# Optimization experiments

Measured on AMD Instinct MI355X. Metric: run time of the kernel, lower is better.

## Reference

```python
import jax, jax.numpy as jnp
import numpy as np

N = 100000   # num nodes
D = 128      # node_emb_dim
R = 8        # num_relations
E = 1600000  # num edges


def setup_inputs() -> dict:
    key = jax.random.key(0)
    k0, k1, k2, k3, k4 = jax.random.split(key, 5)
    x = jax.random.normal(k0, (N, D), dtype=jnp.float32)
    edge_index = jax.random.randint(k1, (2, E), 0, N, dtype=jnp.int32)
    edge_type = jax.random.randint(k2, (E,), 0, R, dtype=jnp.int32)
    scale = 1.0 / np.sqrt(D)
    W = (jax.random.normal(k3, (R, D, D), dtype=jnp.float32) * scale)       # per-relation weight
    W_root = (jax.random.normal(k4, (D, D), dtype=jnp.float32) * scale)     # root (self-loop) weight
    bias = jnp.zeros((D,), dtype=jnp.float32)
    return {"x": x, "W": W, "W_root": W_root, "bias": bias,
            "edge_index": edge_index, "edge_type": edge_type}


def reference(x, W, W_root, bias, edge_index, edge_type):
    # PyG RGCNConv (num_bases=None, aggr='mean', root_weight=True, bias=True):
    # out_i = x_i @ W_root + bias + sum_r mean_{j in N_r(i)} x_j @ W_r
    # Mean aggregation is linear, so aggregate neighbor features per (node, relation)
    # first, then apply the per-relation transform (avoids [E,D,D] intermediates).
    src, dst = edge_index[0], edge_index[1]
    seg = dst * R + edge_type                                   # [E] segment id per (dst, rel)
    cnt = jax.ops.segment_sum(jnp.ones((E,), x.dtype), seg, num_segments=N * R)  # [N*R]
    sums = jax.ops.segment_sum(x[src], seg, num_segments=N * R)                   # [N*R, D]
    mean = sums / jnp.maximum(cnt, 1.0)[:, None]                                  # [N*R, D]
    rel_out = jnp.einsum('nrd,rde->ne', mean.reshape(N, R, D), W)                 # [N, D]
    return rel_out + x @ W_root + bias
```

## Files before the change

### kernel.cpp

```cpp
#include <hip/hip_runtime.h>


constexpr int D = 128;
constexpr int R = 8;
constexpr int TILE = 2048;
constexpr int CW = 64;
constexpr int LDA = 40;

typedef __bf16 bf16x8 __attribute__((ext_vector_type(8)));
typedef float  f32x4  __attribute__((ext_vector_type(4)));
typedef unsigned short u16x8 __attribute__((ext_vector_type(8)));
typedef unsigned short u16x4 __attribute__((ext_vector_type(4)));

__device__ __forceinline__ unsigned short f2bf(float f) {
    unsigned u = __builtin_bit_cast(unsigned, f);
    u += 0x7FFFu + ((u >> 16) & 1u);
    return (unsigned short)(u >> 16);
}
__device__ __forceinline__ float bf2f(unsigned short h) {
    return __builtin_bit_cast(float, (unsigned)h << 16);
}

__global__ __launch_bounds__(256)
void xbf_kernel(const float* __restrict__ x, unsigned short* __restrict__ xbf, int nquad) {
    int stride = gridDim.x * 256;
    for (int i = blockIdx.x * 256 + threadIdx.x; i < nquad; i += stride) {
        float4 v = ((const float4*)x)[i];
        u16x4 o;
        o[0] = f2bf(v.x); o[1] = f2bf(v.y); o[2] = f2bf(v.z); o[3] = f2bf(v.w);
        ((u16x4*)xbf)[i] = o;
    }
}

__global__ __launch_bounds__(256)
void bcount_kernel(const int* __restrict__ dst, const int* __restrict__ et,
                   int* __restrict__ meta, int* __restrict__ hist, int E) {
    __shared__ int cnt8[8];
    if (threadIdx.x < 8) cnt8[threadIdx.x] = 0;
    __syncthreads();
    int stride = gridDim.x * 256;
    for (int e = blockIdx.x * 256 + threadIdx.x; e < E; e += stride) {
        int seg = dst[e] * R + et[e];
        atomicAdd(&cnt8[(seg >> 7) & 7], 1);
        atomicAdd(&hist[seg], 1);
    }
    __syncthreads();
    if (threadIdx.x < 8) atomicAdd(&meta[threadIdx.x], cnt8[threadIdx.x]);
}

__global__ void bscan_kernel(int* __restrict__ meta) {
    if (threadIdx.x == 0) {
        int cum = 0;
        for (int p = 0; p < 8; ++p) {
            meta[8 + p]  = cum;
            meta[16 + p] = cum;
            cum += meta[p];
        }
    }
}

__global__ __launch_bounds__(256)
void bucketA_kernel(const int* __restrict__ src, const int* __restrict__ dst,
                    const int* __restrict__ et, int* __restrict__ ebuf_seg,
                    int* __restrict__ ebuf_src, int* __restrict__ meta, int E) {
    __shared__ int cntw[4][8];
    __shared__ int basew[4][8];
    const int tid = threadIdx.x;
    const int w   = tid >> 6;
    for (int t0 = blockIdx.x * TILE; t0 < E; t0 += gridDim.x * TILE) {
        if (tid < 32) cntw[tid >> 3][tid & 7] = 0;
        __syncthreads();
        int seg[8], sr[8], pt[8];
        bool ok[8];
        #pragma unroll
        for (int j = 0; j < 8; ++j) {
            int e = t0 + j * 256 + tid;
            ok[j] = e < E;
            if (ok[j]) {
                seg[j] = dst[e] * R + et[e];
                sr[j]  = src[e];
                pt[j]  = (seg[j] >> 7) & 7;
                atomicAdd(&cntw[w][pt[j]], 1);
            }
        }
        __syncthreads();
        if (tid < 8) {
            int p = tid;
            int tot = cntw[0][p] + cntw[1][p] + cntw[2][p] + cntw[3][p];
            int b = atomicAdd(&meta[16 + p], tot);
            basew[0][p] = b;               b += cntw[0][p];
            basew[1][p] = b;               b += cntw[1][p];
            basew[2][p] = b;               b += cntw[2][p];
            basew[3][p] = b;
            cntw[0][p] = 0; cntw[1][p] = 0; cntw[2][p] = 0; cntw[3][p] = 0;
        }
        __syncthreads();
        #pragma unroll
        for (int j = 0; j < 8; ++j) {
            if (ok[j]) {
                int r   = atomicAdd(&cntw[w][pt[j]], 1);
                int pos = basew[w][pt[j]] + r;
                ebuf_seg[pos] = seg[j];
                ebuf_src[pos] = sr[j];
            }
        }
        __syncthreads();
    }
}

__global__ __launch_bounds__(256)
void block_sums_kernel(const int* __restrict__ hs, int* __restrict__ bsum, int n) {
    __shared__ int sh[256];
    int i = blockIdx.x * 256 + threadIdx.x;
    sh[threadIdx.x] = (i < n) ? hs[i] : 0;
    __syncthreads();
    for (int off = 128; off > 0; off >>= 1) {
        if (threadIdx.x < off) sh[threadIdx.x] += sh[threadIdx.x + off];
        __syncthreads();
    }
    if (threadIdx.x == 0) bsum[blockIdx.x] = sh[0];
}

__global__ __launch_bounds__(64)
void scan_bsum_kernel(int* __restrict__ bsum, int nb) {
    int lane = threadIdx.x;
    int carry = 0;
    for (int base = 0; base < nb; base += 64) {
        int i = base + lane;
        int orig = (i < nb) ? bsum[i] : 0;
        int v = orig;
        #pragma unroll
        for (int off = 1; off < 64; off <<= 1) {
            int u = __shfl_up(v, off, 64);
            if (lane >= off) v += u;
        }
        int tot = __shfl(v, 63, 64);
        if (i < nb) bsum[i] = carry + (v - orig);
        carry += tot;
    }
}

__global__ __launch_bounds__(256)
void scan_block_kernel(int* __restrict__ hs, const int* __restrict__ bsum,
                       int* __restrict__ cursor, int n, int E) {
    __shared__ int sh[256];
    int tid = threadIdx.x;
    int i = blockIdx.x * 256 + tid;
    int v = (i < n) ? hs[i] : 0;
    sh[tid] = v;
    __syncthreads();
    for (int off = 1; off < 256; off <<= 1) {
        int u = (tid >= off) ? sh[tid - off] : 0;
        __syncthreads();
        sh[tid] += u;
        __syncthreads();
    }
    int st = bsum[blockIdx.x] + sh[tid] - v;
    if (i < n) { hs[i] = st; cursor[i] = st; }
    if (i == n) hs[n] = E;
}

__global__ __launch_bounds__(256)
void bucketB_kernel(const int* __restrict__ ebuf_seg, const int* __restrict__ ebuf_src,
                    const int* __restrict__ meta, int* __restrict__ cursor,
                    int* __restrict__ spack) {
    int part = blockIdx.x & 7;
    int nb   = gridDim.x >> 3;
    int lo   = meta[8 + part];
    int n    = meta[part];
    for (int i = (blockIdx.x >> 3) * 256 + threadIdx.x; i < n; i += nb * 256) {
        int seg = ebuf_seg[lo + i];
        int s   = ebuf_src[lo + i];
        int pos = atomicAdd(&cursor[seg], 1);
        spack[pos] = s;
    }
}

__global__ __launch_bounds__(256)
void aggregate_kernel(const unsigned short* __restrict__ xbf,
                      const int* __restrict__ spack,
                      const int* __restrict__ hstart,
                      unsigned short* __restrict__ mean,
                      int nseg, int c0) {
    int idx = blockIdx.x * 256 + threadIdx.x;
    int seg = idx >> 3;
    int c8  = idx & 7;
    if (seg >= nseg) return;
    int p0 = hstart[seg], p1 = hstart[seg + 1];
    int coff = c0 + c8 * 8;
    float a[8] = {};
    for (int p = p0; p < p1; p += 4) {
        int s0 = spack[p];
        int s1 = (p + 1 < p1) ? spack[p + 1] : -1;
        int s2 = (p + 2 < p1) ? spack[p + 2] : -1;
        int s3 = (p + 3 < p1) ? spack[p + 3] : -1;
        u16x8 v0 = *(const u16x8*)(xbf + ((size_t)s0 << 7) + coff);
        #pragma unroll
        for (int j = 0; j < 8; ++j) a[j] += bf2f(v0[j]);
        if (s1 >= 0) {
            u16x8 v = *(const u16x8*)(xbf + ((size_t)s1 << 7) + coff);
            #pragma unroll
            for (int j = 0; j < 8; ++j) a[j] += bf2f(v[j]);
        }
        if (s2 >= 0) {
            u16x8 v = *(const u16x8*)(xbf + ((size_t)s2 << 7) + coff);
            #pragma unroll
            for (int j = 0; j < 8; ++j) a[j] += bf2f(v[j]);
        }
        if (s3 >= 0) {
            u16x8 v = *(const u16x8*)(xbf + ((size_t)s3 << 7) + coff);
            #pragma unroll
            for (int j = 0; j < 8; ++j) a[j] += bf2f(v[j]);
        }
    }
    float inv = (p1 > p0) ? 1.0f / (float)(p1 - p0) : 0.0f;
    u16x8 o;
    #pragma unroll
    for (int j = 0; j < 8; ++j) o[j] = f2bf(a[j] * inv);
    *(u16x8*)(mean + ((size_t)seg << 6) + c8 * 8) = o;
}

__global__ __launch_bounds__(256)
void wallt_kernel(const float* __restrict__ Wroot, const float* __restrict__ W,
                  unsigned short* __restrict__ WallTc, int KW, int c0, int first) {
    int idx = blockIdx.x * 256 + threadIdx.x;
    if (idx >= 128 * KW) return;
    int n = idx / KW, kk = idx % KW;
    float v;
    if (first && kk < 128) {
        v = Wroot[kk * 128 + n];
    } else {
        int lk = kk - (first ? 128 : 0);
        int r = lk / CW, cc = lk % CW;
        v = W[((size_t)r * 128 + c0 + cc) * 128 + n];
    }
    WallTc[idx] = f2bf(v);
}

template<bool FIRST>
__global__ __launch_bounds__(256)
void mfma_gemm_kernel(const unsigned short* __restrict__ xbf,
                      const unsigned short* __restrict__ mean,
                      const unsigned short* __restrict__ WallTc,
                      const float* __restrict__ bias,
                      float* __restrict__ out,
                      int N, int NT, int KW, int MROW) {
    __shared__ unsigned short As[64 * LDA];
    __shared__ unsigned short Bs[128 * LDA];
    const int tid  = threadIdx.x;
    const int nd0  = blockIdx.x * 64;
    const int lane = tid & 63;
    const int wid  = tid >> 6;
    const int wm   = wid >> 1;
    const int wn   = wid & 1;
    const int arow = tid >> 2;
    const int aoct = tid & 3;
    const int brow = tid >> 1;
    const int bhalf = tid & 1;

    f32x4 acc[2][4] = {};

    const int  anode = nd0 + arow;
    const bool aok   = anode < N;

    for (int kt = 0; kt < NT; ++kt) {
        if (kt) __syncthreads();
        u16x8 av8;
        #pragma unroll
        for (int j = 0; j < 8; ++j) av8[j] = 0;
        if (aok) {
            if (FIRST && kt < 4)
                av8 = *(const u16x8*)(xbf + ((size_t)anode << 7) + kt * 32 + aoct * 8);
            else
                av8 = *(const u16x8*)(mean + (size_t)anode * MROW
                                      + (kt - (FIRST ? 4 : 0)) * 32 + aoct * 8);
        }
        const u16x8* wp = (const u16x8*)(WallTc + (size_t)brow * KW + kt * 32 + bhalf * 16);
        u16x8 b0 = wp[0], b1 = wp[1];

        *(u16x8*)&As[arow * LDA + aoct * 8]            = av8;
        *(u16x8*)&Bs[brow * LDA + bhalf * 16]          = b0;
        *(u16x8*)&Bs[brow * LDA + bhalf * 16 + 8]      = b1;
        __syncthreads();

        const int ko = (lane >> 4) * 8;
        const int rl = lane & 15;
        bf16x8 af[2], bf[4];
        #pragma unroll
        for (int f = 0; f < 2; ++f)
            af[f] = __builtin_bit_cast(bf16x8,
                *(const u16x8*)&As[(wm * 32 + f * 16 + rl) * LDA + ko]);
        #pragma unroll
        for (int f = 0; f < 4; ++f)
            bf[f] = __builtin_bit_cast(bf16x8,
                *(const u16x8*)&Bs[(wn * 64 + f * 16 + rl) * LDA + ko]);
        #pragma unroll
        for (int mf = 0; mf < 2; ++mf)
            #pragma unroll
            for (int nf = 0; nf < 4; ++nf)
                acc[mf][nf] = __builtin_amdgcn_mfma_f32_16x16x32_bf16(af[mf], bf[nf],
                                                                     acc[mf][nf], 0, 0, 0);
    }

    const int rl = lane & 15;
    const int rg = lane >> 4;
    #pragma unroll
    for (int nf = 0; nf < 4; ++nf) {
        int n = wn * 64 + nf * 16 + rl;
        float bb = FIRST ? bias[n] : 0.0f;
        #pragma unroll
        for (int mf = 0; mf < 2; ++mf) {
            #pragma unroll
            for (int i = 0; i < 4; ++i) {
                int nd = nd0 + wm * 32 + mf * 16 + rg * 4 + i;
                if (nd < N) {
                    size_t o = (size_t)nd * 128 + n;
                    if (FIRST) out[o] = acc[mf][nf][i] + bb;
                    else       out[o] += acc[mf][nf][i];
                }
            }
        }
    }
}

extern "C" void kernel_launch(void* const* d_in, const int* in_sizes, int n_in,
                              void* d_out, int out_size, void* d_ws, size_t ws_size,
                              hipStream_t stream) {
    const float* x     = (const float*)d_in[0];
    const float* W     = (const float*)d_in[1];
    const float* Wroot = (const float*)d_in[2];
    const float* bias  = (const float*)d_in[3];
    const int*   ei    = (const int*)d_in[4];
    const int*   et    = (const int*)d_in[5];
    float*       out   = (float*)d_out;

    const int N = in_sizes[0] / D;
    const int E = in_sizes[5];
    const int* src = ei;
    const int* dst = ei + E;

    const int NSEG = N * R;
    const int NB   = (NSEG + 256) / 256;

    const size_t mean_bytes   = (size_t)NSEG * CW * 2;
    const size_t xbf_bytes    = (size_t)N * D * 2;
    const size_t walltc_bytes = (size_t)128 * 640 * 2;
    const size_t need = mean_bytes + xbf_bytes + walltc_bytes +
                        ((size_t)(NSEG + 1) + NSEG + E + NB + 32 + 2 * (size_t)E) * 4 + 256;
    if (ws_size < need) return;

    char* p = (char*)d_ws;
    unsigned short* mean   = (unsigned short*)p;  p += mean_bytes;
    unsigned short* xbf    = (unsigned short*)p;  p += xbf_bytes;
    unsigned short* WallTc = (unsigned short*)p;  p += walltc_bytes;
    int* hstart   = (int*)p;  p += (size_t)(NSEG + 1) * 4;
    int* cursor   = (int*)p;  p += (size_t)NSEG * 4;
    int* spack    = (int*)p;  p += (size_t)E * 4;
    int* bsum     = (int*)p;  p += (size_t)NB * 4;
    int* meta     = (int*)p;  p += 32 * 4;
    int* ebuf_seg = (int*)p;  p += (size_t)E * 4;
    int* ebuf_src = (int*)p;

    hipMemsetAsync(hstart, 0, (size_t)(NSEG + 1) * 4, stream);
    hipMemsetAsync(meta, 0, 32 * 4, stream);

    xbf_kernel<<<2048, 256, 0, stream>>>(x, xbf, N * D / 4);

    bcount_kernel<<<1024, 256, 0, stream>>>(dst, et, meta, hstart, E);
    bscan_kernel<<<1, 64, 0, stream>>>(meta);
    bucketA_kernel<<<(E + TILE - 1) / TILE, 256, 0, stream>>>(
        src, dst, et, ebuf_seg, ebuf_src, meta, E);
    block_sums_kernel<<<NB, 256, 0, stream>>>(hstart, bsum, NSEG);
    scan_bsum_kernel<<<1, 64, 0, stream>>>(bsum, NB);
    scan_block_kernel<<<NB, 256, 0, stream>>>(hstart, bsum, cursor, NSEG, E);
    bucketB_kernel<<<768, 256, 0, stream>>>(ebuf_seg, ebuf_src, meta, cursor, spack);

    const int gx = (N + 63) / 64;
    for (int c = 0; c < 2; ++c) {
        int c0    = c * CW;
        int first = (c == 0);
        aggregate_kernel<<<(NSEG * 8 + 255) / 256, 256, 0, stream>>>(
            xbf, spack, hstart, mean, NSEG, c0);
        int KW   = (first ? 128 : 0) + R * CW;
        int NT   = KW / 32;
        int MROW = R * CW;
        wallt_kernel<<<(128 * KW + 255) / 256, 256, 0, stream>>>(
            Wroot, W, WallTc, KW, c0, first);
        if (first)
            mfma_gemm_kernel<true><<<gx, 256, 0, stream>>>(
                xbf, mean, WallTc, bias, out, N, NT, KW, MROW);
        else
            mfma_gemm_kernel<false><<<gx, 256, 0, stream>>>(
                xbf, mean, WallTc, bias, out, N, NT, KW, MROW);
    }
}
```

Measured before the change: 416.6 us.

## Fuse conversion and bucket count, build histogram from bucketed edges, single weight transpose

```diff
diff --git a/kernel.cpp b/kernel.cpp
--- a/kernel.cpp
+++ b/kernel.cpp
@@ -21,31 +21,32 @@
     return __builtin_bit_cast(float, (unsigned)h << 16);
 }
 
-__global__ __launch_bounds__(256)
-void xbf_kernel(const float* __restrict__ x, unsigned short* __restrict__ xbf, int nquad) {
-    int stride = gridDim.x * 256;
-    for (int i = blockIdx.x * 256 + threadIdx.x; i < nquad; i += stride) {
-        float4 v = ((const float4*)x)[i];
-        u16x4 o;
-        o[0] = f2bf(v.x); o[1] = f2bf(v.y); o[2] = f2bf(v.z); o[3] = f2bf(v.w);
-        ((u16x4*)xbf)[i] = o;
-    }
-}
-
-__global__ __launch_bounds__(256)
-void bcount_kernel(const int* __restrict__ dst, const int* __restrict__ et,
-                   int* __restrict__ meta, int* __restrict__ hist, int E) {
-    __shared__ int cnt8[8];
-    if (threadIdx.x < 8) cnt8[threadIdx.x] = 0;
-    __syncthreads();
-    int stride = gridDim.x * 256;
-    for (int e = blockIdx.x * 256 + threadIdx.x; e < E; e += stride) {
-        int seg = dst[e] * R + et[e];
-        atomicAdd(&cnt8[(seg >> 7) & 7], 1);
-        atomicAdd(&hist[seg], 1);
-    }
-    __syncthreads();
-    if (threadIdx.x < 8) atomicAdd(&meta[threadIdx.x], cnt8[threadIdx.x]);
+constexpr int XB = 768;
+constexpr int CB = 512;
+__global__ __launch_bounds__(256)
+void pre_kernel(const float* __restrict__ x, unsigned short* __restrict__ xbf, int nquad,
+                const int* __restrict__ dst, const int* __restrict__ et,
+                int* __restrict__ meta, int E) {
+    if (blockIdx.x < XB) {
+        int stride = XB * 256;
+        for (int i = blockIdx.x * 256 + threadIdx.x; i < nquad; i += stride) {
+            float4 v = ((const float4*)x)[i];
+            u16x4 o;
+            o[0] = f2bf(v.x); o[1] = f2bf(v.y); o[2] = f2bf(v.z); o[3] = f2bf(v.w);
+            ((u16x4*)xbf)[i] = o;
+        }
+    } else {
+        __shared__ int cnt8[8];
+        if (threadIdx.x < 8) cnt8[threadIdx.x] = 0;
+        __syncthreads();
+        int stride = CB * 256;
+        for (int e = (blockIdx.x - XB) * 256 + threadIdx.x; e < E; e += stride) {
+            int seg = dst[e] * R + et[e];
+            atomicAdd(&cnt8[(seg >> 7) & 7], 1);
+        }
+        __syncthreads();
+        if (threadIdx.x < 8) atomicAdd(&meta[threadIdx.x], cnt8[threadIdx.x]);
+    }
 }
 
 __global__ void bscan_kernel(int* __restrict__ meta) {
@@ -106,6 +107,17 @@
         }
         __syncthreads();
     }
+}
+
+__global__ __launch_bounds__(256)
+void hist_kernel(const int* __restrict__ ebuf_seg, const int* __restrict__ meta,
+                 int* __restrict__ hist) {
+    int part = blockIdx.x & 7;
+    int nb   = gridDim.x >> 3;
+    int lo   = meta[8 + part];
+    int n    = meta[part];
+    for (int i = (blockIdx.x >> 3) * 256 + threadIdx.x; i < n; i += nb * 256)
+        atomicAdd(&hist[ebuf_seg[lo + i]], 1);
 }
 
 __global__ __launch_bounds__(256)
@@ -222,18 +234,12 @@
 
 __global__ __launch_bounds__(256)
 void wallt_kernel(const float* __restrict__ Wroot, const float* __restrict__ W,
-                  unsigned short* __restrict__ WallTc, int KW, int c0, int first) {
+                  unsigned short* __restrict__ WallTc) {
     int idx = blockIdx.x * 256 + threadIdx.x;
-    if (idx >= 128 * KW) return;
-    int n = idx / KW, kk = idx % KW;
-    float v;
-    if (first && kk < 128) {
-        v = Wroot[kk * 128 + n];
-    } else {
-        int lk = kk - (first ? 128 : 0);
-        int r = lk / CW, cc = lk % CW;
-        v = W[((size_t)r * 128 + c0 + cc) * 128 + n];
-    }
+    if (idx >= 128 * 1152) return;
+    int n = idx / 1152, k = idx % 1152;
+    float v = (k < 1024) ? W[(size_t)(k >> 7) * 16384 + (size_t)(k & 127) * 128 + n]
+                         : Wroot[(size_t)(k - 1024) * 128 + n];
     WallTc[idx] = f2bf(v);
 }
 
@@ -244,7 +250,8 @@
                       const unsigned short* __restrict__ WallTc,
                       const float* __restrict__ bias,
                       float* __restrict__ out,
-                      int N, int NT, int KW, int MROW) {
+                      int N, int c0) {
+    constexpr int NT = FIRST ? 20 : 16;
     __shared__ unsigned short As[64 * LDA];
     __shared__ unsigned short Bs[128 * LDA];
     const int tid  = threadIdx.x;
@@ -268,19 +275,23 @@
         u16x8 av8;
         #pragma unroll
         for (int j = 0; j < 8; ++j) av8[j] = 0;
-        if (aok) {
-            if (FIRST && kt < 4)
+        int kbase;
+        if (FIRST && kt < 4) {
+            if (aok)
                 av8 = *(const u16x8*)(xbf + ((size_t)anode << 7) + kt * 32 + aoct * 8);
-            else
-                av8 = *(const u16x8*)(mean + (size_t)anode * MROW
-                                      + (kt - (FIRST ? 4 : 0)) * 32 + aoct * 8);
-        }
-        const u16x8* wp = (const u16x8*)(WallTc + (size_t)brow * KW + kt * 32 + bhalf * 16);
+            kbase = 1024 + kt * 32;
+        } else {
+            int lk = (kt - (FIRST ? 4 : 0)) * 32;
+            if (aok)
+                av8 = *(const u16x8*)(mean + ((size_t)anode << 9) + lk + aoct * 8);
+            kbase = (lk >> 6) * 128 + c0 + (lk & 63);
+        }
+        const u16x8* wp = (const u16x8*)(WallTc + (size_t)brow * 1152 + kbase + bhalf * 16);
         u16x8 b0 = wp[0], b1 = wp[1];
 
-        *(u16x8*)&As[arow * LDA + aoct * 8]            = av8;
-        *(u16x8*)&Bs[brow * LDA + bhalf * 16]          = b0;
-        *(u16x8*)&Bs[brow * LDA + bhalf * 16 + 8]      = b1;
+        *(u16x8*)&As[arow * LDA + aoct * 8]       = av8;
+        *(u16x8*)&Bs[brow * LDA + bhalf * 16]     = b0;
+        *(u16x8*)&Bs[brow * LDA + bhalf * 16 + 8] = b1;
         __syncthreads();
 
         const int ko = (lane >> 4) * 8;
@@ -344,7 +355,7 @@
 
     const size_t mean_bytes   = (size_t)NSEG * CW * 2;
     const size_t xbf_bytes    = (size_t)N * D * 2;
-    const size_t walltc_bytes = (size_t)128 * 640 * 2;
+    const size_t walltc_bytes = (size_t)128 * 1152 * 2;
     const size_t need = mean_bytes + xbf_bytes + walltc_bytes +
                         ((size_t)(NSEG + 1) + NSEG + E + NB + 32 + 2 * (size_t)E) * 4 + 256;
     if (ws_size < need) return;
@@ -364,33 +375,28 @@
     hipMemsetAsync(hstart, 0, (size_t)(NSEG + 1) * 4, stream);
     hipMemsetAsync(meta, 0, 32 * 4, stream);
 
-    xbf_kernel<<<2048, 256, 0, stream>>>(x, xbf, N * D / 4);
-
-    bcount_kernel<<<1024, 256, 0, stream>>>(dst, et, meta, hstart, E);
+    pre_kernel<<<XB + CB, 256, 0, stream>>>(x, xbf, N * D / 4, dst, et, meta, E);
     bscan_kernel<<<1, 64, 0, stream>>>(meta);
     bucketA_kernel<<<(E + TILE - 1) / TILE, 256, 0, stream>>>(
         src, dst, et, ebuf_seg, ebuf_src, meta, E);
+    hist_kernel<<<768, 256, 0, stream>>>(ebuf_seg, meta, hstart);
     block_sums_kernel<<<NB, 256, 0, stream>>>(hstart, bsum, NSEG);
     scan_bsum_kernel<<<1, 64, 0, stream>>>(bsum, NB);
     scan_block_kernel<<<NB, 256, 0, stream>>>(hstart, bsum, cursor, NSEG, E);
     bucketB_kernel<<<768, 256, 0, stream>>>(ebuf_seg, ebuf_src, meta, cursor, spack);
 
+    wallt_kernel<<<(128 * 1152 + 255) / 256, 256, 0, stream>>>(Wroot, W, WallTc);
+
     const int gx = (N + 63) / 64;
     for (int c = 0; c < 2; ++c) {
-        int c0    = c * CW;
-        int first = (c == 0);
+        int c0 = c * CW;
         aggregate_kernel<<<(NSEG * 8 + 255) / 256, 256, 0, stream>>>(
             xbf, spack, hstart, mean, NSEG, c0);
-        int KW   = (first ? 128 : 0) + R * CW;
-        int NT   = KW / 32;
-        int MROW = R * CW;
-        wallt_kernel<<<(128 * KW + 255) / 256, 256, 0, stream>>>(
-            Wroot, W, WallTc, KW, c0, first);
-        if (first)
+        if (c == 0)
             mfma_gemm_kernel<true><<<gx, 256, 0, stream>>>(
-                xbf, mean, WallTc, bias, out, N, NT, KW, MROW);
+                xbf, mean, WallTc, bias, out, N, c0);
         else
             mfma_gemm_kernel<false><<<gx, 256, 0, stream>>>(
-                xbf, mean, WallTc, bias, out, N, NT, KW, MROW);
-    }
-}
+                xbf, mean, WallTc, bias, out, N, c0);
+    }
+}
```

Result: no change. 416.7 us (+0.0%).
